# Performance work log

Measured on AMD Instinct MI355X. Metric: run time of the kernel, lower is better.

The kernel has to match this reference:

```python
import jax, jax.numpy as jnp
import numpy as np

N = 50000
E = 1600000

def _glorot(key, shape):
    fan_in, fan_out = shape[0], shape[1]
    lim = jnp.sqrt(6.0 / (fan_in + fan_out))
    return jax.random.uniform(key, shape, jnp.float32, -lim, lim)

def setup_inputs() -> dict:
    key = jax.random.key(0)
    ks = jax.random.split(key, 20)
    inp = {
        "x": jax.random.normal(ks[0], (N, 128), jnp.float32),
        "gx": jax.random.normal(ks[1], (N, 128), jnp.float32),
        "edge_index": jax.random.randint(ks[2], (2, E), 0, N, jnp.int64),
        # edgeconv1: Linear(256, 128)
        "W1": _glorot(ks[3], (256, 128)), "b1": jnp.zeros((128,), jnp.float32),
        # dimreduc: Linear(128, 128)
        "Wdr": _glorot(ks[4], (128, 128)), "bdr": jnp.zeros((128,), jnp.float32),
        # gcnconv1: GCNConv(128, 128)
        "Wg1": _glorot(ks[5], (128, 128)), "bg1": jnp.zeros((128,), jnp.float32),
        # gcnconv2: GCNConv(128, 128)
        "Wg2": _glorot(ks[6], (128, 128)), "bg2": jnp.zeros((128,), jnp.float32),
        # edgeconv2: Linear(384, 128)
        "W2": _glorot(ks[7], (384, 128)), "b2": jnp.zeros((128,), jnp.float32),
        # edgeconv3: Linear(128, 64)
        "W3": _glorot(ks[8], (128, 64)), "b3": jnp.zeros((64,), jnp.float32),
        # out: Linear(64, 10)
        "Wo": _glorot(ks[9], (64, 10)), "bo": jnp.zeros((10,), jnp.float32),
    }
    return inp

def gcn_conv(x, W, b, src, dst, n):
    # PyG GCNConv: out = D^{-1/2}(A+I)D^{-1/2} (x @ W) + b, with self-loops added
    h = x @ W                                     # [N, F_out]
    loops = jnp.arange(n, dtype=src.dtype)
    s = jnp.concatenate([src, loops])             # sources with self-loops
    d = jnp.concatenate([dst, loops])             # targets with self-loops
    ones = jnp.ones(s.shape[0], x.dtype)
    deg = jax.ops.segment_sum(ones, d, num_segments=n)   # in-degree incl. self-loop
    dinv = jnp.where(deg > 0, jax.lax.rsqrt(deg), 0.0)
    norm = dinv[s] * dinv[d]                      # [E+N]
    msg = h[s] * norm[:, None]                    # gather + scale
    out = jax.ops.segment_sum(msg, d, num_segments=n)    # scatter-add
    return out + b

def reference(x, gx, edge_index, W1, b1, Wdr, bdr, Wg1, bg1, Wg2, bg2, W2, b2, W3, b3, Wo, bo):
    src, dst = edge_index[0], edge_index[1]
    n = x.shape[0]
    z = jax.nn.relu(jnp.concatenate([x, gx], axis=1) @ W1 + b1)   # [N,128]
    z0 = z @ Wdr + bdr                                            # [N,128]
    z1 = jax.nn.relu(gcn_conv(z + gx, Wg1, bg1, src, dst, n))     # [N,128]
    z2 = jax.nn.relu(gcn_conv(z1, Wg2, bg2, src, dst, n))         # [N,128]
    z = jax.nn.relu(jnp.concatenate([z, z1, z2], axis=1) @ W2 + b2)  # [N,128]
    z = jax.nn.relu((z + z0) @ W3 + b3)                           # [N,64]
    return z @ Wo + bo                                            # [N,10]
```

## Files before the change

kernel.cpp:

```cpp
#include <hip/hip_runtime.h>

typedef __attribute__((ext_vector_type(4))) float f32x4;
typedef __attribute__((ext_vector_type(2))) float f32x2;
typedef __attribute__((ext_vector_type(8))) short bf16x8;
typedef __attribute__((ext_vector_type(4))) int i32x4;

#define HIST_RANGE 16384

__device__ __forceinline__ unsigned short bf16_rne(float f) {
    unsigned int u = __float_as_uint(f);
    u += 0x7fffu + ((u >> 16) & 1u);
    return (unsigned short)(u >> 16);
}

__device__ __forceinline__ void split_bf16(float f, unsigned short& hi, unsigned short& lo) {
    unsigned int u = __float_as_uint(f);
    hi = (unsigned short)(u >> 16);
    float r = f - __uint_as_float((unsigned int)hi << 16);
    lo = (unsigned short)(__float_as_uint(r) >> 16);
}

__device__ __forceinline__ unsigned char fp8_e4m3(float f) {
    int p = __builtin_amdgcn_cvt_pk_fp8_f32(f, 0.f, 0, false);
    return (unsigned char)(p & 0xff);
}


__global__ void k_detect(const unsigned int* ei, int* flag) {
    if (blockIdx.x == 0 && threadIdx.x == 0) {
        int is64 = 1;
        for (int i = 0; i < 64; ++i) {
            if (ei[2 * i + 1] != 0u) { is64 = 0; break; }
        }
        *flag = is64;
    }
}

__global__ void k_convert(const void* ei, int twoE, const int* flag, int* __restrict__ out) {
    int p = blockIdx.x * blockDim.x + threadIdx.x;
    int b = p * 2;
    if (b + 1 < twoE) {
        if (*flag) {
            i32x4 v = *(const i32x4*)((const long long*)ei + b);
            int2 o; o.x = v.x; o.y = v.z;
            *(int2*)(out + b) = o;
        } else {
            *(int2*)(out + b) = *(const int2*)((const int*)ei + b);
        }
    } else if (b < twoE) {
        out[b] = (*flag) ? (int)((const long long*)ei)[b] : ((const int*)ei)[b];
    }
}

__global__ void k_hist_atomic(const int* __restrict__ dst, int E, int* __restrict__ cnt) {
    int e = blockIdx.x * blockDim.x + threadIdx.x;
    if (e < E) atomicAdd(&cnt[dst[e]], 1);
}


__global__ __launch_bounds__(256) void k_hist_part(
    const int* __restrict__ dst, int E, int n, int nrep, unsigned short* __restrict__ partial)
{
    __shared__ int h[HIST_RANGE];
    const int cls = blockIdx.x & 3;
    const int rep = blockIdx.x >> 2;
    const int range = (n + 3) >> 2;
    const int lo = cls * range;
    const int hi = min(n, lo + range);
    const int cr = hi - lo;
    if (cr <= 0) return;
    for (int i = threadIdx.x; i < cr; i += 256) h[i] = 0;
    __syncthreads();
    const int chunk = (((E + nrep - 1) / nrep) + 2047) & ~2047;
    const int ebeg = rep * chunk;
    const int eend = min(E, ebeg + chunk);
    if ((E & 3) == 0) {
        for (int e = ebeg + (int)threadIdx.x * 4; e < eend; e += 2048) {
            i32x4 da = __builtin_nontemporal_load((const i32x4*)(dst + e));
            int e2 = e + 1024;
            bool has2 = e2 < eend;
            i32x4 db;
            if (has2) db = __builtin_nontemporal_load((const i32x4*)(dst + e2));
            if (da.x >= lo && da.x < hi) atomicAdd(&h[da.x - lo], 1);
            if (da.y >= lo && da.y < hi) atomicAdd(&h[da.y - lo], 1);
            if (da.z >= lo && da.z < hi) atomicAdd(&h[da.z - lo], 1);
            if (da.w >= lo && da.w < hi) atomicAdd(&h[da.w - lo], 1);
            if (has2) {
                if (db.x >= lo && db.x < hi) atomicAdd(&h[db.x - lo], 1);
                if (db.y >= lo && db.y < hi) atomicAdd(&h[db.y - lo], 1);
                if (db.z >= lo && db.z < hi) atomicAdd(&h[db.z - lo], 1);
                if (db.w >= lo && db.w < hi) atomicAdd(&h[db.w - lo], 1);
            }
        }
    } else {
        for (int e = ebeg + (int)threadIdx.x; e < eend; e += 256) {
            int d = __builtin_nontemporal_load(&dst[e]);
            if (d >= lo && d < hi) atomicAdd(&h[d - lo], 1);
        }
    }
    __syncthreads();
    unsigned short* po = partial + (size_t)rep * n + lo;
    for (int i = threadIdx.x; i < cr; i += 256) po[i] = (unsigned short)h[i];
}


__global__ __launch_bounds__(512) void k_scan1(
    const unsigned short* __restrict__ partial, int nrep, int n,
    int* __restrict__ cnt, int* __restrict__ rowptr, int* __restrict__ bsum,
    unsigned short* __restrict__ base)
{
    __shared__ int part[512];
    const int t = threadIdx.x;
    const int i = blockIdx.x * 512 + t;
    int own = 0;
    if (i < n) {
        for (int r = 0; r < nrep; ++r) {
            base[(size_t)r * n + i] = (unsigned short)own;
            own += partial[(size_t)r * n + i];
        }
        cnt[i] = own;
    }
    part[t] = own;
    __syncthreads();
#pragma unroll
    for (int off = 1; off < 512; off <<= 1) {
        int v = (t >= off) ? part[t - off] : 0;
        __syncthreads();
        part[t] += v;
        __syncthreads();
    }
    if (i < n) rowptr[i] = part[t] - own;
    if (t == 511) bsum[blockIdx.x] = part[511];
}

__global__ __launch_bounds__(256) void k_scan2(const int* __restrict__ bsum, int nb,
                                               int* __restrict__ bofs) {
    __shared__ int part[256];
    const int t = threadIdx.x;
    int own = (t < nb) ? bsum[t] : 0;
    part[t] = own;
    __syncthreads();
#pragma unroll
    for (int off = 1; off < 256; off <<= 1) {
        int v = (t >= off) ? part[t - off] : 0;
        __syncthreads();
        part[t] += v;
        __syncthreads();
    }
    if (t < nb) bofs[t] = part[t] - own;
}

__global__ void k_scan3(const int* __restrict__ cnt, int n, int E,
                        const int* __restrict__ bofs, int* __restrict__ rowptr,
                        int* __restrict__ cursor, float* __restrict__ dinv) {
    int i = blockIdx.x * blockDim.x + threadIdx.x;
    if (i >= n) return;
    int rp = rowptr[i] + bofs[i >> 9];
    rowptr[i] = rp;
    cursor[i] = rp;
    dinv[i] = rsqrtf((float)(cnt[i] + 1));
    if (i == 0) rowptr[n] = E;
}


__global__ __launch_bounds__(256) void k_fill_np(
    const int* __restrict__ src, const int* __restrict__ dst, int E, int n, int nrep,
    const int* __restrict__ rowptr, const unsigned short* __restrict__ base,
    int* __restrict__ csr)
{
    __shared__ int cur[HIST_RANGE];
    const int cls = blockIdx.x & 3;
    const int rep = blockIdx.x >> 2;
    const int range = (n + 3) >> 2;
    const int lo = cls * range;
    const int hi = min(n, lo + range);
    const int cr = hi - lo;
    if (cr <= 0) return;
    const unsigned short* bp = base + (size_t)rep * n + lo;
    for (int i = threadIdx.x; i < cr; i += 256) cur[i] = rowptr[lo + i] + (int)bp[i];
    __syncthreads();
    const int chunk = (((E + nrep - 1) / nrep) + 2047) & ~2047;
    const int ebeg = rep * chunk;
    const int eend = min(E, ebeg + chunk);
    if ((E & 3) == 0) {
        for (int e = ebeg + (int)threadIdx.x * 4; e < eend; e += 2048) {
            i32x4 da = __builtin_nontemporal_load((const i32x4*)(dst + e));
            int e2 = e + 1024;
            bool has2 = e2 < eend;
            i32x4 db;
            if (has2) db = __builtin_nontemporal_load((const i32x4*)(dst + e2));
            {
                bool m0 = da.x >= lo && da.x < hi;
                bool m1 = da.y >= lo && da.y < hi;
                bool m2 = da.z >= lo && da.z < hi;
                bool m3 = da.w >= lo && da.w < hi;
                if (m0 | m1 | m2 | m3) {
                    i32x4 s4 = __builtin_nontemporal_load((const i32x4*)(src + e));
                    if (m0) { int p = atomicAdd(&cur[da.x - lo], 1); csr[p] = s4.x; }
                    if (m1) { int p = atomicAdd(&cur[da.y - lo], 1); csr[p] = s4.y; }
                    if (m2) { int p = atomicAdd(&cur[da.z - lo], 1); csr[p] = s4.z; }
                    if (m3) { int p = atomicAdd(&cur[da.w - lo], 1); csr[p] = s4.w; }
                }
            }
            if (has2) {
                bool m0 = db.x >= lo && db.x < hi;
                bool m1 = db.y >= lo && db.y < hi;
                bool m2 = db.z >= lo && db.z < hi;
                bool m3 = db.w >= lo && db.w < hi;
                if (m0 | m1 | m2 | m3) {
                    i32x4 s4 = __builtin_nontemporal_load((const i32x4*)(src + e2));
                    if (m0) { int p = atomicAdd(&cur[db.x - lo], 1); csr[p] = s4.x; }
                    if (m1) { int p = atomicAdd(&cur[db.y - lo], 1); csr[p] = s4.y; }
                    if (m2) { int p = atomicAdd(&cur[db.z - lo], 1); csr[p] = s4.z; }
                    if (m3) { int p = atomicAdd(&cur[db.w - lo], 1); csr[p] = s4.w; }
                }
            }
        }
    } else {
        for (int e = ebeg + (int)threadIdx.x; e < eend; e += 256) {
            int d = __builtin_nontemporal_load(&dst[e]);
            if (d >= lo && d < hi) {
                int s = __builtin_nontemporal_load(&src[e]);
                int p = atomicAdd(&cur[d - lo], 1);
                csr[p] = s;
            }
        }
    }
}

__global__ __launch_bounds__(256) void k_fill_part(
    const int* __restrict__ src, const int* __restrict__ dst, int E, int n,
    int* __restrict__ cursor, int* __restrict__ csr)
{
    const int range = blockIdx.x & 7;
    const int chunk = blockIdx.x >> 3;
    const int nchunks = gridDim.x >> 3;
    const int lo = (int)(((long long)n * range) >> 3);
    const int hi = (int)(((long long)n * (range + 1)) >> 3);
    for (int e = chunk * 256 + (int)threadIdx.x; e < E; e += nchunks * 256) {
        int d = __builtin_nontemporal_load(&dst[e]);
        if (d >= lo && d < hi) {
            int s = __builtin_nontemporal_load(&src[e]);
            int pos = atomicAdd(&cursor[d], 1);
            csr[pos] = s;
        }
    }
}


__global__ __launch_bounds__(256) void k_split2(const float* __restrict__ x,
                                                const float* __restrict__ gx,
                                                unsigned short* __restrict__ Ox,
                                                unsigned short* __restrict__ Og, int n8) {
    int i = blockIdx.x * blockDim.x + threadIdx.x;
    const float* in; unsigned short* O; int k;
    if (i < n8) { in = x; O = Ox; k = i; }
    else if (i < 2 * n8) { in = gx; O = Og; k = i - n8; }
    else return;
    f32x4 v0 = ((const f32x4*)in)[k * 2];
    f32x4 v1 = ((const f32x4*)in)[k * 2 + 1];
    bf16x8 o;
#pragma unroll
    for (int j = 0; j < 8; ++j) {
        float f = (j < 4) ? v0[j] : v1[j - 4];
        o[j] = (short)bf16_rne(f);
    }
    *(bf16x8*)(O + (size_t)k * 8) = o;
}


struct WCArgs {
    const float* W[6];
    unsigned short* WH[6];
    unsigned short* WL[6];
    int K[6], F[6];
    int tofs[7];
};

__global__ __launch_bounds__(256) void k_wconv_all(WCArgs a) {
    int idx = blockIdx.x * blockDim.x + threadIdx.x;
    if (idx >= a.tofs[6]) return;
    int s = 0;
    while (idx >= a.tofs[s + 1]) ++s;
    int t0 = idx - a.tofs[s];
    const float* W = a.W[s];
    int K = a.K[s], F = a.F[s];
    int lane = t0 & 63;
    int t = t0 >> 6;
    int CT = F / 16;
    int ks = t / CT, ct = t % CT;
    int col = ct * 16 + (lane & 15);
    int kbase = ks * 32 + (lane >> 4) * 8;
    bf16x8 h, l;
#pragma unroll
    for (int j = 0; j < 8; ++j) {
        unsigned short hi, lo;
        split_bf16(W[(size_t)(kbase + j) * F + col], hi, lo);
        h[j] = (short)hi; l[j] = (short)lo;
    }
    *(bf16x8*)(a.WH[s] + (size_t)t0 * 8) = h;
    *(bf16x8*)(a.WL[s] + (size_t)t0 * 8) = l;
}


__device__ __forceinline__ void stage_load(const unsigned short* Ap, int row0, int n, int tid,
                                           bf16x8& s0, bf16x8& s1) {
    int row = tid >> 3;
    int cb = (tid & 7) << 5;
    int gr = min(row0 + row, n - 1);
    const char* gp = (const char*)Ap + ((size_t)gr << 8) + cb;
    s0 = *(const bf16x8*)gp;
    s1 = *(const bf16x8*)(gp + 16);
}

__device__ __forceinline__ void stage_write(unsigned short* td, int tid, bf16x8 s0, bf16x8 s1) {
    int row = tid >> 3;
    int cb = (tid & 7) << 5;
    int s = (row & 7) << 4;
    char* t = (char*)td + row * 256;
    *(bf16x8*)(t + (cb ^ s)) = s0;
    *(bf16x8*)(t + ((cb + 16) ^ s)) = s1;
}

template<int K, int F, int EPI, bool RELU, bool BIAS, bool SUM2, bool POSTADD>
__global__ __launch_bounds__(256, 3) void k_sgemm(
    const unsigned short* __restrict__ A0, const unsigned short* __restrict__ A1,
    const unsigned short* __restrict__ A2,
    const unsigned short* __restrict__ WH, const unsigned short* __restrict__ WL,
    const float* __restrict__ bias, const float* __restrict__ post,
    const float* __restrict__ dinv, void* __restrict__ o1, int n)
{
    constexpr int CT = F / 16;
    constexpr int CTW = CT / 4;
    constexpr int NCH = K / 128;
    __shared__ unsigned short tile[2][32 * 128];
    const int tid = threadIdx.x;
    const int lane = tid & 63;
    const int wave = tid >> 6;
    const int row0 = blockIdx.x * 32;
    const int arow = lane & 15;
    const int kgrp = lane >> 4;

    f32x4 acc[2][CTW];
#pragma unroll
    for (int rt = 0; rt < 2; ++rt)
#pragma unroll
        for (int c = 0; c < CTW; ++c) acc[rt][c] = (f32x4)(0.f);

    bf16x8 p0, p1;
    stage_load(A0, row0, n, tid, p0, p1);
    stage_write(tile[0], tid, p0, p1);
    if constexpr (SUM2) {
        stage_load(A1, row0, n, tid, p0, p1);
        stage_write(tile[1], tid, p0, p1);
    }

#pragma unroll
    for (int ch = 0; ch < NCH; ++ch) {
        __syncthreads();
        if (ch + 1 < NCH) {
            const unsigned short* Apn = (ch + 1 == 1) ? A1 : A2;
            stage_load(Apn, row0, n, tid, p0, p1);
        }
        bf16x8 bh[4][CTW], bl[4][CTW];
#pragma unroll
        for (int ks = 0; ks < 4; ++ks)
#pragma unroll
            for (int c = 0; c < CTW; ++c) {
                int ct = wave * CTW + c;
                size_t fo = (((size_t)(ch * 4 + ks) * CT + ct) * 64 + lane) * 8;
                bh[ks][c] = *(const bf16x8*)(WH + fo);
                bl[ks][c] = *(const bf16x8*)(WL + fo);
            }
        int tsrc = SUM2 ? 0 : (ch & 1);
        bf16x8 a[2][4];
#pragma unroll
        for (int rt = 0; rt < 2; ++rt)
#pragma unroll
            for (int ks = 0; ks < 4; ++ks) {
                int row = rt * 16 + arow;
                int cb = (ks * 64 + kgrp * 16) ^ ((row & 7) << 4);
                a[rt][ks] = *(const bf16x8*)((const char*)tile[tsrc] + row * 256 + cb);
            }
        bf16x8 a2f[2][4];
        if constexpr (SUM2) {
#pragma unroll
            for (int rt = 0; rt < 2; ++rt)
#pragma unroll
                for (int ks = 0; ks < 4; ++ks) {
                    int row = rt * 16 + arow;
                    int cb = (ks * 64 + kgrp * 16) ^ ((row & 7) << 4);
                    a2f[rt][ks] = *(const bf16x8*)((const char*)tile[1] + row * 256 + cb);
                }
        }
#pragma unroll
        for (int ks = 0; ks < 4; ++ks)
#pragma unroll
            for (int c = 0; c < CTW; ++c)
#pragma unroll
                for (int rt = 0; rt < 2; ++rt) {
                    acc[rt][c] = __builtin_amdgcn_mfma_f32_16x16x32_bf16(a[rt][ks], bh[ks][c], acc[rt][c], 0, 0, 0);
                    acc[rt][c] = __builtin_amdgcn_mfma_f32_16x16x32_bf16(a[rt][ks], bl[ks][c], acc[rt][c], 0, 0, 0);
                    if constexpr (SUM2) {
                        acc[rt][c] = __builtin_amdgcn_mfma_f32_16x16x32_bf16(a2f[rt][ks], bh[ks][c], acc[rt][c], 0, 0, 0);
                        acc[rt][c] = __builtin_amdgcn_mfma_f32_16x16x32_bf16(a2f[rt][ks], bl[ks][c], acc[rt][c], 0, 0, 0);
                    }
                }
        if (ch + 1 < NCH) stage_write(tile[(ch + 1) & 1], tid, p0, p1);
    }

    if constexpr (EPI == 1) {
        unsigned char* ob = (unsigned char*)o1;
        float dv[2][4];
#pragma unroll
        for (int rt = 0; rt < 2; ++rt)
#pragma unroll
            for (int r = 0; r < 4; ++r) {
                int row = row0 + rt * 16 + kgrp * 4 + r;
                dv[rt][r] = (row < n) ? dinv[row] : 0.f;
            }
#pragma unroll
        for (int rt = 0; rt < 2; ++rt)
#pragma unroll
            for (int c = 0; c < CTW; ++c) {
                int j = (wave * CTW + c) * 16 + arow;
#pragma unroll
                for (int r = 0; r < 4; ++r) {
                    int row = row0 + rt * 16 + kgrp * 4 + r;
                    if (row < n) ob[(size_t)row * F + j] = fp8_e4m3(acc[rt][c][r] * dv[rt][r]);
                }
            }
    } else if constexpr (EPI == 2) {
        unsigned short* ob = (unsigned short*)o1;
#pragma unroll
        for (int rt = 0; rt < 2; ++rt)
#pragma unroll
            for (int c = 0; c < CTW; ++c) {
                int j = (wave * CTW + c) * 16 + arow;
                float bv = 0.f;
                if constexpr (BIAS) bv = bias[j];
#pragma unroll
                for (int r = 0; r < 4; ++r) {
                    int row = row0 + rt * 16 + kgrp * 4 + r;
                    if (row < n) {
                        float v = acc[rt][c][r];
                        if constexpr (BIAS) v += bv;
                        if constexpr (RELU) v = fmaxf(v, 0.f);
                        if constexpr (POSTADD) v += post[(size_t)row * F + j];
                        ob[(size_t)row * F + j] = bf16_rne(v);
                    }
                }
            }
    } else {
        float* ofp = (float*)o1;
#pragma unroll
        for (int rt = 0; rt < 2; ++rt)
#pragma unroll
            for (int c = 0; c < CTW; ++c) {
                int j = (wave * CTW + c) * 16 + arow;
                float bv = 0.f;
                if constexpr (BIAS) bv = bias[j];
#pragma unroll
                for (int r = 0; r < 4; ++r) {
                    int row = row0 + rt * 16 + kgrp * 4 + r;
                    if (row < n) {
                        float v = acc[rt][c][r];
                        if constexpr (BIAS) v += bv;
                        if constexpr (RELU) v = fmaxf(v, 0.f);
                        if constexpr (POSTADD) v += post[(size_t)row * F + j];
                        ofp[(size_t)row * F + j] = v;
                    }
                }
            }
    }
}


#define ACCW(w) { f32x2 lo_ = __builtin_amdgcn_cvt_pk_f32_fp8((int)(w), false); \
                  f32x2 hi_ = __builtin_amdgcn_cvt_pk_f32_fp8((int)(w), true);  \
                  a0 += lo_.x; a1 += lo_.y; a2 += hi_.x; a3 += hi_.y; }

__global__ __launch_bounds__(256) void k_agg_bf(
    const int* __restrict__ rowptr, const int* __restrict__ csr,
    const float* __restrict__ dinv, const unsigned char* __restrict__ hs,
    const float* __restrict__ bias, unsigned short* __restrict__ outB, int n)
{
    const int node = blockIdx.x * 8 + (threadIdx.x >> 5);
    if (node >= n) return;
    const int c = threadIdx.x & 31;
    const float dd = dinv[node];
    const int beg = rowptr[node];
    const int end = rowptr[node + 1];
    const unsigned int* hw = (const unsigned int*)hs;

    float a0 = 0.f, a1 = 0.f, a2 = 0.f, a3 = 0.f;
    {
        unsigned int w = hw[(size_t)node * 32 + c];
        ACCW(w)
    }

    int j = beg;
    for (; j + 7 < end; j += 8) {
        int s0 = csr[j],     s1 = csr[j + 1], s2 = csr[j + 2], s3 = csr[j + 3];
        int s4 = csr[j + 4], s5 = csr[j + 5], s6 = csr[j + 6], s7 = csr[j + 7];
        unsigned int w0 = hw[(size_t)s0 * 32 + c];
        unsigned int w1 = hw[(size_t)s1 * 32 + c];
        unsigned int w2 = hw[(size_t)s2 * 32 + c];
        unsigned int w3 = hw[(size_t)s3 * 32 + c];
        unsigned int w4 = hw[(size_t)s4 * 32 + c];
        unsigned int w5 = hw[(size_t)s5 * 32 + c];
        unsigned int w6 = hw[(size_t)s6 * 32 + c];
        unsigned int w7 = hw[(size_t)s7 * 32 + c];
        ACCW(w0) ACCW(w1) ACCW(w2) ACCW(w3)
        ACCW(w4) ACCW(w5) ACCW(w6) ACCW(w7)
    }
    for (; j + 3 < end; j += 4) {
        int s0 = csr[j], s1 = csr[j + 1], s2 = csr[j + 2], s3 = csr[j + 3];
        unsigned int w0 = hw[(size_t)s0 * 32 + c];
        unsigned int w1 = hw[(size_t)s1 * 32 + c];
        unsigned int w2 = hw[(size_t)s2 * 32 + c];
        unsigned int w3 = hw[(size_t)s3 * 32 + c];
        ACCW(w0) ACCW(w1) ACCW(w2) ACCW(w3)
    }
    for (; j < end; ++j) {
        unsigned int w = hw[(size_t)csr[j] * 32 + c];
        ACCW(w)
    }

    float4 bv = ((const float4*)bias)[c];
    ushort4 h4;
    h4.x = bf16_rne(fmaxf(fmaf(dd, a0, bv.x), 0.f));
    h4.y = bf16_rne(fmaxf(fmaf(dd, a1, bv.y), 0.f));
    h4.z = bf16_rne(fmaxf(fmaf(dd, a2, bv.z), 0.f));
    h4.w = bf16_rne(fmaxf(fmaf(dd, a3, bv.w), 0.f));
    *(ushort4*)(outB + (size_t)node * 128 + c * 4) = h4;
}


__global__ __launch_bounds__(256) void k_final(const float* __restrict__ z7, const float* __restrict__ Wo,
                        const float* __restrict__ bo, float* __restrict__ out, int n) {
    __shared__ float Wos[64][10];
    __shared__ float bos[10];
    if (threadIdx.x < 64) {
#pragma unroll
        for (int j = 0; j < 10; ++j) Wos[threadIdx.x][j] = Wo[threadIdx.x * 10 + j];
        if (threadIdx.x < 10) bos[threadIdx.x] = bo[threadIdx.x];
    }
    __syncthreads();
    int idx = blockIdx.x * blockDim.x + threadIdx.x;
    if (idx >= n * 10) return;
    int row = idx / 10, j = idx % 10;
    const float* zr = z7 + (size_t)row * 64;
    float acc = bos[j];
#pragma unroll
    for (int k = 0; k < 64; ++k) acc = fmaf(zr[k], Wos[k][j], acc);
    out[idx] = acc;
}


extern "C" void kernel_launch(void* const* d_in, const int* in_sizes, int n_in,
                              void* d_out, int out_size, void* d_ws, size_t ws_size,
                              hipStream_t stream) {
    const float* x   = (const float*)d_in[0];
    const float* gx  = (const float*)d_in[1];
    const void*  ei  = d_in[2];
    const float* W1  = (const float*)d_in[3];  const float* b1  = (const float*)d_in[4];
    const float* Wdr = (const float*)d_in[5];  const float* bdr = (const float*)d_in[6];
    const float* Wg1 = (const float*)d_in[7];  const float* bg1 = (const float*)d_in[8];
    const float* Wg2 = (const float*)d_in[9];  const float* bg2 = (const float*)d_in[10];
    const float* W2  = (const float*)d_in[11]; const float* b2  = (const float*)d_in[12];
    const float* W3  = (const float*)d_in[13]; const float* b3  = (const float*)d_in[14];
    const float* Wo  = (const float*)d_in[15]; const float* bo  = (const float*)d_in[16];
    float* out = (float*)d_out;
    const int n = in_sizes[0] / 128;
    const int E = in_sizes[2] / 2;
    const int twoE = 2 * E;
    const int nb = (n + 511) / 512;
    const int NREP = 128;

    char* ws = (char*)d_ws;
    size_t off = 0;
    auto alloc = [&](size_t bytes) -> void* {
        void* p = ws + off;
        off = (off + bytes + 255) & ~(size_t)255;
        return p;
    };
    int*   flag   = (int*)  alloc(256);
    int*   cnt    = (int*)  alloc((size_t)n * 4);
    int*   rowptr = (int*)  alloc(((size_t)n + 1) * 4);
    int*   cursor = (int*)  alloc((size_t)n * 4);
    float* dinv   = (float*)alloc((size_t)n * 4);
    int*   bsum   = (int*)  alloc(1024);
    int*   bofs   = (int*)  alloc(1024);
    int*   es     = (int*)  alloc((size_t)twoE * 4);
    int*   ed     = es + E;
    int*   csr    = (int*)  alloc((size_t)E * 4);
    unsigned short* W1H  = (unsigned short*)alloc(256 * 128 * 2);
    unsigned short* W1L  = (unsigned short*)alloc(256 * 128 * 2);
    unsigned short* WdrH = (unsigned short*)alloc(128 * 128 * 2);
    unsigned short* WdrL = (unsigned short*)alloc(128 * 128 * 2);
    unsigned short* Wg1H = (unsigned short*)alloc(128 * 128 * 2);
    unsigned short* Wg1L = (unsigned short*)alloc(128 * 128 * 2);
    unsigned short* Wg2H = (unsigned short*)alloc(128 * 128 * 2);
    unsigned short* Wg2L = (unsigned short*)alloc(128 * 128 * 2);
    unsigned short* W2H  = (unsigned short*)alloc(384 * 128 * 2);
    unsigned short* W2L  = (unsigned short*)alloc(384 * 128 * 2);
    unsigned short* W3H  = (unsigned short*)alloc(128 * 64 * 2);
    unsigned short* W3L  = (unsigned short*)alloc(128 * 64 * 2);
    const size_t nf = (size_t)n * 128;
    unsigned short* XaB = (unsigned short*)alloc(nf * 2);
    unsigned short* XgB = (unsigned short*)alloc(nf * 2);
    size_t prep_bytes = 2 * ((size_t)NREP * n * 2 + 256);
    size_t act_bytes  = (nf * 2 + 256) * 2 + (nf + 256) + (nf * 4 + 256);
    char* arena = (char*)alloc(prep_bytes > act_bytes ? prep_bytes : act_bytes);
    unsigned short* partial = (unsigned short*)arena;
    unsigned short* base    = (unsigned short*)(arena + (((size_t)NREP * n * 2 + 255) & ~(size_t)255));
    char* ap = arena;
    auto carve = [&](size_t bytes) -> void* {
        void* p = ap;
        ap += (bytes + 255) & ~(size_t)255;
        return p;
    };
    unsigned short* ZB  = (unsigned short*)carve(nf * 2);
    unsigned short* Z1B = (unsigned short*)carve(nf * 2);
    unsigned char*  HS  = (unsigned char*) carve(nf);
    float* B1 = (float*)carve(nf * 4);
    unsigned short* TB  = XaB;
    unsigned short* Z2B = XgB;
    unsigned char*  HS2 = HS;
    (void)ws_size; (void)n_in; (void)out_size;

    k_detect<<<1, 64, 0, stream>>>((const unsigned int*)ei, flag);
    k_convert<<<(twoE / 2 + 255) / 256, 256, 0, stream>>>(ei, twoE, flag, es);
    if (n <= 4 * HIST_RANGE) {
        k_hist_part<<<4 * NREP, 256, 0, stream>>>(ed, E, n, NREP, partial);
        k_scan1<<<nb, 512, 0, stream>>>(partial, NREP, n, cnt, rowptr, bsum, base);
        k_scan2<<<1, 256, 0, stream>>>(bsum, nb, bofs);
        k_scan3<<<(n + 255) / 256, 256, 0, stream>>>(cnt, n, E, bofs, rowptr, cursor, dinv);
        k_fill_np<<<4 * NREP, 256, 0, stream>>>(es, ed, E, n, NREP, rowptr, base, csr);
    } else {
        hipMemsetAsync(cnt, 0, (size_t)n * 4, stream);
        k_hist_atomic<<<(E + 255) / 256, 256, 0, stream>>>(ed, E, cnt);
        k_scan1<<<nb, 512, 0, stream>>>((const unsigned short*)nullptr, 0, n, cnt, rowptr, bsum, base);
        k_scan2<<<1, 256, 0, stream>>>(bsum, nb, bofs);
        k_scan3<<<(n + 255) / 256, 256, 0, stream>>>(cnt, n, E, bofs, rowptr, cursor, dinv);
        k_fill_part<<<2048, 256, 0, stream>>>(es, ed, E, n, cursor, csr);
    }

    {
        WCArgs a;
        const float* Ws[6] = { W1, Wdr, Wg1, Wg2, W2, W3 };
        unsigned short* WHs[6] = { W1H, WdrH, Wg1H, Wg2H, W2H, W3H };
        unsigned short* WLs[6] = { W1L, WdrL, Wg1L, Wg2L, W2L, W3L };
        int Ks[6] = { 256, 128, 128, 128, 384, 128 };
        int Fs[6] = { 128, 128, 128, 128, 128, 64 };
        int acc = 0;
        for (int s = 0; s < 6; ++s) {
            a.W[s] = Ws[s]; a.WH[s] = WHs[s]; a.WL[s] = WLs[s];
            a.K[s] = Ks[s]; a.F[s] = Fs[s];
            a.tofs[s] = acc;
            acc += Ks[s] * Fs[s] / 8;
        }
        a.tofs[6] = acc;
        k_wconv_all<<<(acc + 255) / 256, 256, 0, stream>>>(a);
    }
    const int n8 = n * 16;
    k_split2<<<(2 * n8 + 255) / 256, 256, 0, stream>>>(x, gx, XaB, XgB, n8);

    const int gm = (n + 31) / 32;
    const int ga = (n + 7) / 8;
    k_sgemm<256, 128, 2, true,  true,  false, false><<<gm, 256, 0, stream>>>(
        XaB, XgB, nullptr, W1H, W1L, b1, nullptr, nullptr, ZB, n);
    k_sgemm<128, 128, 0, false, true,  false, false><<<gm, 256, 0, stream>>>(
        ZB, nullptr, nullptr, WdrH, WdrL, bdr, nullptr, nullptr, B1, n);
    k_sgemm<128, 128, 1, false, false, true,  false><<<gm, 256, 0, stream>>>(
        ZB, XgB, nullptr, Wg1H, Wg1L, nullptr, nullptr, dinv, HS, n);
    k_agg_bf<<<ga, 256, 0, stream>>>(rowptr, csr, dinv, HS, bg1, Z1B, n);
    k_sgemm<128, 128, 1, false, false, false, false><<<gm, 256, 0, stream>>>(
        Z1B, nullptr, nullptr, Wg2H, Wg2L, nullptr, nullptr, dinv, HS2, n);
    k_agg_bf<<<ga, 256, 0, stream>>>(rowptr, csr, dinv, HS2, bg2, Z2B, n);
    k_sgemm<384, 128, 2, true,  true,  false, true ><<<gm, 256, 0, stream>>>(
        ZB, Z1B, Z2B, W2H, W2L, b2, B1, nullptr, TB, n);
    k_sgemm<128, 64,  0, true,  true,  false, false><<<gm, 256, 0, stream>>>(
        TB, nullptr, nullptr, W3H, W3L, b3, nullptr, nullptr, B1, n);
    k_final<<<(n * 10 + 255) / 256, 256, 0, stream>>>(B1, Wo, bo, out, n);
}
```

Measured before the change: 265.3 us.

## Fuse dimreduc and GCN1 GEMMs into one kernel sharing the ZB tile

Adds a dual GEMM kernel that loads the ZB and gx row tiles once and computes both z@Wdr+bdr and (z+gx)@Wg1 scaled by dinv. This replaces two separate GEMM launches and one redundant read of ZB. The z0 intermediate is now stored as bf16 rather than fp32, which roughly halves its write and its later read in the W2 epilogue, at some precision cost. The fused kernel needs more registers, so launch bounds drop to 2 blocks per unit.

```diff
diff --git a/kernel.cpp b/kernel.cpp
--- a/kernel.cpp
+++ b/kernel.cpp
@@ -327,7 +327,7 @@
     const unsigned short* __restrict__ A0, const unsigned short* __restrict__ A1,
     const unsigned short* __restrict__ A2,
     const unsigned short* __restrict__ WH, const unsigned short* __restrict__ WL,
-    const float* __restrict__ bias, const float* __restrict__ post,
+    const float* __restrict__ bias, const unsigned short* __restrict__ post,
     const float* __restrict__ dinv, void* __restrict__ o1, int n)
 {
     constexpr int CT = F / 16;
@@ -446,7 +446,8 @@
                         float v = acc[rt][c][r];
                         if constexpr (BIAS) v += bv;
                         if constexpr (RELU) v = fmaxf(v, 0.f);
-                        if constexpr (POSTADD) v += post[(size_t)row * F + j];
+                        if constexpr (POSTADD)
+                            v += __uint_as_float((unsigned int)post[(size_t)row * F + j] << 16);
                         ob[(size_t)row * F + j] = bf16_rne(v);
                     }
                 }
@@ -467,12 +468,97 @@
                         float v = acc[rt][c][r];
                         if constexpr (BIAS) v += bv;
                         if constexpr (RELU) v = fmaxf(v, 0.f);
-                        if constexpr (POSTADD) v += post[(size_t)row * F + j];
                         ofp[(size_t)row * F + j] = v;
                     }
                 }
             }
     }
+}
+
+
+__global__ __launch_bounds__(256, 2) void k_dgemm(
+    const unsigned short* __restrict__ ZB, const unsigned short* __restrict__ XgB,
+    const unsigned short* __restrict__ WdH, const unsigned short* __restrict__ WdL,
+    const unsigned short* __restrict__ WgH, const unsigned short* __restrict__ WgL,
+    const float* __restrict__ bdr, const float* __restrict__ dinv,
+    unsigned short* __restrict__ Z0B, unsigned char* __restrict__ HS, int n)
+{
+    constexpr int F = 128, CT = 8, CTW = 2;
+    __shared__ unsigned short tile[2][32 * 128];
+    const int tid = threadIdx.x;
+    const int lane = tid & 63;
+    const int wave = tid >> 6;
+    const int row0 = blockIdx.x * 32;
+    const int arow = lane & 15;
+    const int kgrp = lane >> 4;
+
+    f32x4 accZ[2][CTW], accH[2][CTW];
+#pragma unroll
+    for (int rt = 0; rt < 2; ++rt)
+#pragma unroll
+        for (int c = 0; c < CTW; ++c) { accZ[rt][c] = (f32x4)(0.f); accH[rt][c] = (f32x4)(0.f); }
+
+    bf16x8 p0, p1;
+    stage_load(ZB, row0, n, tid, p0, p1);
+    stage_write(tile[0], tid, p0, p1);
+    stage_load(XgB, row0, n, tid, p0, p1);
+    stage_write(tile[1], tid, p0, p1);
+    __syncthreads();
+
+    bf16x8 a[2][4], g[2][4];
+#pragma unroll
+    for (int rt = 0; rt < 2; ++rt)
+#pragma unroll
+        for (int ks = 0; ks < 4; ++ks) {
+            int row = rt * 16 + arow;
+            int cb = (ks * 64 + kgrp * 16) ^ ((row & 7) << 4);
+            a[rt][ks] = *(const bf16x8*)((const char*)tile[0] + row * 256 + cb);
+            g[rt][ks] = *(const bf16x8*)((const char*)tile[1] + row * 256 + cb);
+        }
+#pragma unroll
+    for (int ks = 0; ks < 4; ++ks)
+#pragma unroll
+        for (int c = 0; c < CTW; ++c) {
+            int ct = wave * CTW + c;
+            size_t fo = (((size_t)ks * CT + ct) * 64 + lane) * 8;
+            bf16x8 dh = *(const bf16x8*)(WdH + fo);
+            bf16x8 dl = *(const bf16x8*)(WdL + fo);
+            bf16x8 gh = *(const bf16x8*)(WgH + fo);
+            bf16x8 gl = *(const bf16x8*)(WgL + fo);
+#pragma unroll
+            for (int rt = 0; rt < 2; ++rt) {
+                accZ[rt][c] = __builtin_amdgcn_mfma_f32_16x16x32_bf16(a[rt][ks], dh, accZ[rt][c], 0, 0, 0);
+                accZ[rt][c] = __builtin_amdgcn_mfma_f32_16x16x32_bf16(a[rt][ks], dl, accZ[rt][c], 0, 0, 0);
+                accH[rt][c] = __builtin_amdgcn_mfma_f32_16x16x32_bf16(a[rt][ks], gh, accH[rt][c], 0, 0, 0);
+                accH[rt][c] = __builtin_amdgcn_mfma_f32_16x16x32_bf16(a[rt][ks], gl, accH[rt][c], 0, 0, 0);
+                accH[rt][c] = __builtin_amdgcn_mfma_f32_16x16x32_bf16(g[rt][ks], gh, accH[rt][c], 0, 0, 0);
+                accH[rt][c] = __builtin_amdgcn_mfma_f32_16x16x32_bf16(g[rt][ks], gl, accH[rt][c], 0, 0, 0);
+            }
+        }
+
+    float dv[2][4];
+#pragma unroll
+    for (int rt = 0; rt < 2; ++rt)
+#pragma unroll
+        for (int r = 0; r < 4; ++r) {
+            int row = row0 + rt * 16 + kgrp * 4 + r;
+            dv[rt][r] = (row < n) ? dinv[row] : 0.f;
+        }
+#pragma unroll
+    for (int rt = 0; rt < 2; ++rt)
+#pragma unroll
+        for (int c = 0; c < CTW; ++c) {
+            int j = (wave * CTW + c) * 16 + arow;
+            float bv = bdr[j];
+#pragma unroll
+            for (int r = 0; r < 4; ++r) {
+                int row = row0 + rt * 16 + kgrp * 4 + r;
+                if (row < n) {
+                    Z0B[(size_t)row * F + j] = bf16_rne(accZ[rt][c][r] + bv);
+                    HS[(size_t)row * F + j] = fp8_e4m3(accH[rt][c][r] * dv[rt][r]);
+                }
+            }
+        }
 }
 
 
@@ -611,7 +697,7 @@
     unsigned short* XaB = (unsigned short*)alloc(nf * 2);
     unsigned short* XgB = (unsigned short*)alloc(nf * 2);
     size_t prep_bytes = 2 * ((size_t)NREP * n * 2 + 256);
-    size_t act_bytes  = (nf * 2 + 256) * 2 + (nf + 256) + (nf * 4 + 256);
+    size_t act_bytes  = (nf * 2 + 256) * 3 + (nf + 256) + ((size_t)n * 64 * 4 + 256);
     char* arena = (char*)alloc(prep_bytes > act_bytes ? prep_bytes : act_bytes);
     unsigned short* partial = (unsigned short*)arena;
     unsigned short* base    = (unsigned short*)(arena + (((size_t)NREP * n * 2 + 255) & ~(size_t)255));
@@ -623,8 +709,9 @@
     };
     unsigned short* ZB  = (unsigned short*)carve(nf * 2);
     unsigned short* Z1B = (unsigned short*)carve(nf * 2);
+    unsigned short* Z0B = (unsigned short*)carve(nf * 2);
     unsigned char*  HS  = (unsigned char*) carve(nf);
-    float* B1 = (float*)carve(nf * 4);
+    float* B1 = (float*)carve((size_t)n * 64 * 4);
     unsigned short* TB  = XaB;
     unsigned short* Z2B = XgB;
     unsigned char*  HS2 = HS;
@@ -671,16 +758,13 @@
     const int ga = (n + 7) / 8;
     k_sgemm<256, 128, 2, true,  true,  false, false><<<gm, 256, 0, stream>>>(
         XaB, XgB, nullptr, W1H, W1L, b1, nullptr, nullptr, ZB, n);
-    k_sgemm<128, 128, 0, false, true,  false, false><<<gm, 256, 0, stream>>>(
-        ZB, nullptr, nullptr, WdrH, WdrL, bdr, nullptr, nullptr, B1, n);
-    k_sgemm<128, 128, 1, false, false, true,  false><<<gm, 256, 0, stream>>>(
-        ZB, XgB, nullptr, Wg1H, Wg1L, nullptr, nullptr, dinv, HS, n);
+    k_dgemm<<<gm, 256, 0, stream>>>(ZB, XgB, WdrH, WdrL, Wg1H, Wg1L, bdr, dinv, Z0B, HS, n);
     k_agg_bf<<<ga, 256, 0, stream>>>(rowptr, csr, dinv, HS, bg1, Z1B, n);
     k_sgemm<128, 128, 1, false, false, false, false><<<gm, 256, 0, stream>>>(
         Z1B, nullptr, nullptr, Wg2H, Wg2L, nullptr, nullptr, dinv, HS2, n);
     k_agg_bf<<<ga, 256, 0, stream>>>(rowptr, csr, dinv, HS2, bg2, Z2B, n);
     k_sgemm<384, 128, 2, true,  true,  false, true ><<<gm, 256, 0, stream>>>(
-        ZB, Z1B, Z2B, W2H, W2L, b2, B1, nullptr, TB, n);
+        ZB, Z1B, Z2B, W2H, W2L, b2, Z0B, nullptr, TB, n);
     k_sgemm<128, 64,  0, true,  true,  false, false><<<gm, 256, 0, stream>>>(
         TB, nullptr, nullptr, W3H, W3L, b3, nullptr, nullptr, B1, n);
     k_final<<<(n * 10 + 255) / 256, 256, 0, stream>>>(B1, Wo, bo, out, n);
```

Result: faster. 258.3 us (-2.7%).
